# Optimization experiments

Measured on AMD Instinct MI355X. Metric: run time of the kernel, lower is better.

The kernel has to match this reference:

```python
import jax, jax.numpy as jnp
import numpy as np

N, E = 20000, 320000
IN, HID, OUT, EO = 256, 256, 128, 64


def setup_inputs() -> dict:
    key = jax.random.key(0)
    ks = iter(jax.random.split(key, 40))
    w = lambda s: jax.random.normal(next(ks), s, jnp.float32) * 0.05
    inp = {
        "x": jax.random.normal(next(ks), (N, IN), jnp.float32),
        "edge_index": jax.random.randint(next(ks), (2, E), 0, N, jnp.int32),
        "edge_attr": jax.random.uniform(next(ks), (E, 1), jnp.float32),
        # conv1 (IN->IN), conv2 (HID->HID)
        "c1_nw": w((IN, IN)), "c1_ew": w((1, EO)), "c1_new": w((IN + EO, IN)), "c1_b": jnp.zeros((IN,)),
        "c2_nw": w((HID, HID)), "c2_ew": w((1, EO)), "c2_new": w((HID + EO, HID)), "c2_b": jnp.zeros((HID,)),
        # conv3_mean / conv3_logstd (OUT->OUT)
        "cm_nw": w((OUT, OUT)), "cm_ew": w((1, EO)), "cm_new": w((OUT + EO, OUT)), "cm_b": jnp.zeros((OUT,)),
        "cl_nw": w((OUT, OUT)), "cl_ew": w((1, EO)), "cl_new": w((OUT + EO, OUT)), "cl_b": jnp.zeros((OUT,)),
        # linears (stored [in,out])
        "lin1_w": w((IN, HID)), "lin1_b": jnp.zeros((HID,)),
        "lin2_w": w((HID, OUT)), "lin2_b": jnp.zeros((OUT,)),
        "pih_w": w((IN, HID)), "pih_b": jnp.zeros((HID,)),
        "pho_w": w((HID, OUT)), "pho_b": jnp.zeros((OUT,)),
        # batchnorm affine params
        "bn1_g": jnp.ones((IN,)), "bn1_b": jnp.zeros((IN,)),
        "bn2_g": jnp.ones((HID,)), "bn2_b": jnp.zeros((HID,)),
        "bnm_g": jnp.ones((OUT,)), "bnm_b": jnp.zeros((OUT,)),
        "bnl_g": jnp.ones((OUT,)), "bnl_b": jnp.zeros((OUT,)),
    }
    return inp


def _forward(x, edge_index, edge_attr,
             c1_nw, c1_ew, c1_new, c1_b,
             c2_nw, c2_ew, c2_new, c2_b,
             cm_nw, cm_ew, cm_new, cm_b,
             cl_nw, cl_ew, cl_new, cl_b,
             lin1_w, lin1_b, lin2_w, lin2_b,
             pih_w, pih_b, pho_w, pho_b,
             bn1_g, bn1_b, bn2_g, bn2_b,
             bnm_g, bnm_b, bnl_g, bnl_b):
    n = x.shape[0]
    loops = jnp.arange(n, dtype=edge_index.dtype)
    row = jnp.concatenate([edge_index[0], loops])  # source j
    col = jnp.concatenate([edge_index[1], loops])  # target i
    ea = jnp.concatenate([edge_attr, jnp.zeros((n, edge_attr.shape[1]), edge_attr.dtype)], 0)
    deg = jax.ops.segment_sum(jnp.ones_like(col, dtype=x.dtype), col, num_segments=n) + 1e-6
    dis = deg ** -0.5
    norm = dis[row] * dis[col]  # [E+N]

    def gcn(h, nw, ew, new_w, b):
        nm = (h @ nw)[row]                      # gather of x_j @ node_weight
        em = ea @ ew                            # [E+N, EO]
        msg = norm[:, None] * (jnp.concatenate([nm, em], axis=1) @ new_w)
        return jax.ops.segment_sum(msg, col, num_segments=n) + b

    def bn(h, g, b):  # BatchNorm1d, training-mode batch stats, eps 1e-5
        m = h.mean(0)
        v = h.var(0)
        return (h - m) * jax.lax.rsqrt(v + 1e-5) * g + b

    # dropout is identity in eval mode
    x1 = jax.nn.relu(bn(gcn(x, c1_nw, c1_ew, c1_new, c1_b), bn1_g, bn1_b)) + x
    x2 = x1 @ lin1_w + lin1_b
    x2 = jax.nn.relu(bn(gcn(x2, c2_nw, c2_ew, c2_new, c2_b), bn2_g, bn2_b)) + (x1 @ pih_w + pih_b)
    x3 = x2 @ lin2_w + lin2_b
    logstd = bn(gcn(x3, cl_nw, cl_ew, cl_new, cl_b), bnl_g, bnl_b)
    mean = bn(gcn(x3, cm_nw, cm_ew, cm_new, cm_b), bnm_g, bnm_b) + (x2 @ pho_w + pho_b)
    # faithful to source: batch_norm_logstd applied a second time and added
    logstd = logstd + bn(logstd, bnl_g, bnl_b)
    return mean, logstd


def reference(x, edge_index, edge_attr,
              c1_nw, c1_ew, c1_new, c1_b,
              c2_nw, c2_ew, c2_new, c2_b,
              cm_nw, cm_ew, cm_new, cm_b,
              cl_nw, cl_ew, cl_new, cl_b,
              lin1_w, lin1_b, lin2_w, lin2_b,
              pih_w, pih_b, pho_w, pho_b,
              bn1_g, bn1_b, bn2_g, bn2_b,
              bnm_g, bnm_b, bnl_g, bnl_b):
    return _forward(x, edge_index, edge_attr,
                    c1_nw, c1_ew, c1_new, c1_b,
                    c2_nw, c2_ew, c2_new, c2_b,
                    cm_nw, cm_ew, cm_new, cm_b,
                    cl_nw, cl_ew, cl_new, cl_b,
                    lin1_w, lin1_b, lin2_w, lin2_b,
                    pih_w, pih_b, pho_w, pho_b,
                    bn1_g, bn1_b, bn2_g, bn2_b,
                    bnm_g, bnm_b, bnl_g, bnl_b)
```

## Files before the change

### kernel.cpp

```cpp
#include <hip/hip_runtime.h>

#define NN 20000
#define EE 320000
#define ET (EE + NN)

typedef __attribute__((ext_vector_type(8))) short short8v;
typedef __attribute__((ext_vector_type(4))) float float4v;

__device__ __forceinline__ float b2f(unsigned short u) {
  union { float f; unsigned int i; } c; c.i = ((unsigned int)u) << 16; return c.f;
}
__device__ __forceinline__ unsigned short f2bs(float f) {
  union { float f; unsigned int u; } c; c.f = f;
  unsigned int r = c.u + 0x7fffu + ((c.u >> 16) & 1u);
  return (unsigned short)(r >> 16);
}

__global__ void detect_kernel(const unsigned short* __restrict__ x, int* __restrict__ flag) {
  __shared__ int cnt_s;
  if (threadIdx.x == 0) cnt_s = 0;
  __syncthreads();
  int pass = 0;
  for (int j = 0; j < 16; ++j) {
    unsigned short u = x[2 * (threadIdx.x * 16 + j)];
    int e = (u >> 7) & 0xFF;
    if (e >= 96 && e <= 150) pass++;
  }
  atomicAdd(&cnt_s, pass);
  __syncthreads();
  if (threadIdx.x == 0) *flag = (cnt_s < 2458) ? 1 : 0;
}

__global__ void convert_kernel(const void* __restrict__ in, float* __restrict__ out, int n4,
                               const int* __restrict__ flag) {
  int i = blockIdx.x * 256 + threadIdx.x;
  if (i >= n4) return;
  if (*flag) {
    ((float4*)out)[i] = ((const float4*)in)[i];
  } else {
    ushort4 u = ((const ushort4*)in)[i];
    ((float4*)out)[i] = make_float4(b2f(u.x), b2f(u.y), b2f(u.z), b2f(u.w));
  }
}

__global__ void convert_x_kernel(const void* __restrict__ in,
                                 short* __restrict__ xh, short* __restrict__ xl, int n4,
                                 const int* __restrict__ flag) {
  int i = blockIdx.x * 256 + threadIdx.x;
  if (i >= n4) return;
  float4 v;
  if (*flag) {
    v = ((const float4*)in)[i];
  } else {
    ushort4 u = ((const ushort4*)in)[i];
    v = make_float4(b2f(u.x), b2f(u.y), b2f(u.z), b2f(u.w));
  }
  ushort4 h, l;
  h.x = f2bs(v.x); l.x = f2bs(v.x - b2f(h.x));
  h.y = f2bs(v.y); l.y = f2bs(v.y - b2f(h.y));
  h.z = f2bs(v.z); l.z = f2bs(v.z - b2f(h.z));
  h.w = f2bs(v.w); l.w = f2bs(v.w - b2f(h.w));
  ((ushort4*)xh)[i] = h;
  ((ushort4*)xl)[i] = l;
}

struct WSpec { const void* p[28]; int off[28]; int len[28]; };
__global__ void convert_weights(WSpec ws, float* __restrict__ out, const int* __restrict__ flag) {
  int b = blockIdx.x;
  int f32m = *flag;
  const void* p = ws.p[b];
  int off = ws.off[b], len4 = ws.len[b] >> 2;
  float4* dst = (float4*)(out + off);
  for (int i = blockIdx.y * 256 + threadIdx.x; i < len4; i += 8 * 256) {
    if (f32m) {
      dst[i] = ((const float4*)p)[i];
    } else {
      ushort4 u = ((const ushort4*)p)[i];
      dst[i] = make_float4(b2f(u.x), b2f(u.y), b2f(u.z), b2f(u.w));
    }
  }
}

__global__ void bconv_kernel(const float* __restrict__ W, int ldb,
                             short* __restrict__ Bh, short* __restrict__ Bl, int N) {
  int idx = blockIdx.x * 256 + threadIdx.x;
  if (idx >= N * 256) return;
  int n = idx >> 8, k = idx & 255;
  float v = W[(size_t)k * ldb + n];
  unsigned short h = f2bs(v);
  size_t o = ((size_t)(k >> 3) * N + n) * 8 + (k & 7);
  Bh[o] = (short)h;
  Bl[o] = (short)f2bs(v - b2f(h));
}

__global__ void count_kernel(const int* __restrict__ ei, int* __restrict__ cnt) {
  int e = blockIdx.x * 256 + threadIdx.x;
  if (e >= ET) return;
  int dst = (e < EE) ? ei[EE + e] : (e - EE);
  atomicAdd(&cnt[dst], 1);
}

__global__ void dis_kernel(const int* __restrict__ cnt, float* __restrict__ dis) {
  int i = blockIdx.x * 256 + threadIdx.x;
  if (i >= NN) return;
  dis[i] = rsqrtf((float)cnt[i] + 1e-6f);
}

__global__ void scan1_kernel(const int* __restrict__ cnt, int* __restrict__ partial,
                             int* __restrict__ bsum) {
  __shared__ int sd[256];
  int b = blockIdx.x, t = threadIdx.x;
  int i = b * 256 + t;
  sd[t] = (i < NN) ? cnt[i] : 0;
  __syncthreads();
  for (int off = 1; off < 256; off <<= 1) {
    int x = (t >= off) ? sd[t - off] : 0;
    __syncthreads();
    sd[t] += x;
    __syncthreads();
  }
  if (i < NN) partial[i] = sd[t];
  if (t == 255) bsum[b] = sd[255];
}

__global__ void scan2_kernel(int* __restrict__ bsum, int nb) {
  __shared__ int sd[128];
  int t = threadIdx.x;
  sd[t] = (t < nb) ? bsum[t] : 0;
  __syncthreads();
  for (int off = 1; off < 128; off <<= 1) {
    int x = (t >= off) ? sd[t - off] : 0;
    __syncthreads();
    sd[t] += x;
    __syncthreads();
  }
  if (t < nb) bsum[t] = sd[t];
}

__global__ void scan3_kernel(const int* __restrict__ partial, const int* __restrict__ bsum,
                             int* __restrict__ rowptr) {
  int i = blockIdx.x * 256 + threadIdx.x;
  if (i == 0) rowptr[0] = 0;
  if (i < NN) {
    int b = i >> 8;
    rowptr[i + 1] = partial[i] + (b ? bsum[b - 1] : 0);
  }
}

__global__ void fill_kernel(const int* __restrict__ ei, const float* __restrict__ eaf,
                            const float* __restrict__ dis, const int* __restrict__ rowptr,
                            int* __restrict__ cursor, int2* __restrict__ csr,
                            float* __restrict__ sarr) {
  int e = blockIdx.x * 256 + threadIdx.x;
  if (e >= ET) return;
  int src, dst; float a;
  if (e < EE) { src = ei[e]; dst = ei[EE + e]; a = eaf[e]; }
  else { src = dst = e - EE; a = 0.f; }
  float coef = dis[src] * dis[dst];
  int pos = rowptr[dst] + atomicAdd(&cursor[dst], 1);
  csr[pos] = make_int2(src, __float_as_int(coef));
  if (a != 0.f) atomicAdd(&sarr[dst], coef * a);
}

struct GJobs {
  const float* A[8]; const float* B[8]; float* C[8];
  int M[8], N[8], K[8], ldc[8], blkx[8], cum[8];
  int njobs;
};
__global__ __launch_bounds__(256) void gemm64_multi(GJobs jb) {
  int bid = blockIdx.x;
  int j = 0;
  while (j < jb.njobs - 1 && bid >= jb.cum[j]) ++j;
  int local = bid - (j ? jb.cum[j - 1] : 0);
  const float* A = jb.A[j];
  const float* B = jb.B[j];
  float* C = jb.C[j];
  int M = jb.M[j], N = jb.N[j], K = jb.K[j], ldc = jb.ldc[j];
  int bx = local % jb.blkx[j], by = local / jb.blkx[j];

  __shared__ float As[16][68];
  __shared__ float Bs[16][64];
  int tid = threadIdx.x;
  int row0 = bx * 64, col0 = by * 64;
  int tr = tid >> 4, tc = tid & 15;
  float acc[4][4] = {};
  int lmA = tid >> 2;
  int lkA = (tid & 3) << 2;
  int lkB = tid >> 4;
  int lcB = (tid & 15) << 2;
  for (int k0 = 0; k0 < K; k0 += 16) {
    int gr = row0 + lmA;
    float4 a4 = make_float4(0.f, 0.f, 0.f, 0.f);
    if (gr < M) a4 = *reinterpret_cast<const float4*>(&A[(size_t)gr * K + k0 + lkA]);
    As[lkA + 0][lmA] = a4.x;
    As[lkA + 1][lmA] = a4.y;
    As[lkA + 2][lmA] = a4.z;
    As[lkA + 3][lmA] = a4.w;
    float4 b4 = *reinterpret_cast<const float4*>(&B[(size_t)(k0 + lkB) * N + col0 + lcB]);
    *reinterpret_cast<float4*>(&Bs[lkB][lcB]) = b4;
    __syncthreads();
#pragma unroll
    for (int kk = 0; kk < 16; ++kk) {
      float4 av = *reinterpret_cast<const float4*>(&As[kk][tr << 2]);
      float4 bv = *reinterpret_cast<const float4*>(&Bs[kk][tc << 2]);
      float aa[4] = {av.x, av.y, av.z, av.w};
      float bb[4] = {bv.x, bv.y, bv.z, bv.w};
#pragma unroll
      for (int i = 0; i < 4; ++i)
#pragma unroll
        for (int jj = 0; jj < 4; ++jj) acc[i][jj] += aa[i] * bb[jj];
    }
    __syncthreads();
  }
#pragma unroll
  for (int i = 0; i < 4; ++i) {
    int gr = row0 + (tr << 2) + i;
    if (gr >= M) continue;
#pragma unroll
    for (int jj = 0; jj < 4; ++jj)
      C[(size_t)gr * ldc + col0 + (tc << 2) + jj] = acc[i][jj];
  }
}

__global__ void copy_strided(const float* __restrict__ src, float* __restrict__ dst,
                             int n, int cshift, int cmask, int ldd) {
  int idx = blockIdx.x * 256 + threadIdx.x;
  if (idx >= n) return;
  int r = idx >> cshift, c = idx & cmask;
  dst[(size_t)r * ldd + c] = src[idx];
}

#define LOADB(ntv, ktv, BH, BL)                                     \
  {                                                                 \
    int n_ = (ntv) * 128 + w * 16 + lm;                             \
    _Pragma("unroll") for (int ks = 0; ks < 2; ++ks) {              \
      int kc = (ktv) * 8 + ks * 4 + lg;                             \
      size_t o = ((size_t)kc * N + n_) * 8;                         \
      BH[ks] = *reinterpret_cast<const short8v*>(Bh + o);           \
      BL[ks] = *reinterpret_cast<const short8v*>(Bl + o);           \
    }                                                               \
  }

__global__ __launch_bounds__(512) void gemm_mfma4(const short* __restrict__ Ah,
                                                  const short* __restrict__ Al,
                                                  const short* __restrict__ Bh,
                                                  const short* __restrict__ Bl,
                                                  unsigned short* __restrict__ C,
                                                  const float* __restrict__ bias,
                                                  int M, int N, int ldc) {
  __shared__ __align__(16) short lds[16384];
  const int K = 256;
  int tid = threadIdx.x;
  int w = tid >> 6, l = tid & 63;
  int row0 = blockIdx.x * 32;
  int lm = l & 15, lg = l >> 4;

#pragma unroll
  for (int i = 0; i < 2; ++i) {
    int id = i * 512 + tid;
    int r = id >> 5, c = id & 31;
    int gr = row0 + r; if (gr >= M) gr = M - 1;
    int sw = c ^ r;
    *reinterpret_cast<float4*>(lds + r * 256 + sw * 8) =
        *reinterpret_cast<const float4*>(Ah + (size_t)gr * K + c * 8);
    *reinterpret_cast<float4*>(lds + 8192 + r * 256 + sw * 8) =
        *reinterpret_cast<const float4*>(Al + (size_t)gr * K + c * 8);
  }
  __syncthreads();

  int NT = N >> 7;
  short8v bhX[2], blX[2], bhY[2], blY[2];
  LOADB(0, 0, bhX, blX);
  for (int nt = 0; nt < NT; ++nt) {
    float4v acc[2] = {};
    int n = nt * 128 + w * 16 + lm;
#pragma unroll
    for (int kt = 0; kt < 4; ++kt) {
      int nt_n = (kt == 3) ? ((nt + 1 < NT) ? nt + 1 : nt) : nt;
      int kt_n = (kt + 1) & 3;
      short8v a_h[2][2], a_l[2][2];
#pragma unroll
      for (int mf = 0; mf < 2; ++mf)
#pragma unroll
        for (int ks = 0; ks < 2; ++ks) {
          int r = mf * 16 + lm;
          int c = kt * 8 + ks * 4 + lg;
          int sw = c ^ r;
          a_h[mf][ks] = *reinterpret_cast<const short8v*>(lds + r * 256 + sw * 8);
          a_l[mf][ks] = *reinterpret_cast<const short8v*>(lds + 8192 + r * 256 + sw * 8);
        }
      if ((kt & 1) == 0) {
        LOADB(nt_n, kt_n, bhY, blY);
#pragma unroll
        for (int mf = 0; mf < 2; ++mf)
#pragma unroll
          for (int ks = 0; ks < 2; ++ks) {
            acc[mf] = __builtin_amdgcn_mfma_f32_16x16x32_bf16(a_h[mf][ks], bhX[ks], acc[mf], 0, 0, 0);
            acc[mf] = __builtin_amdgcn_mfma_f32_16x16x32_bf16(a_h[mf][ks], blX[ks], acc[mf], 0, 0, 0);
            acc[mf] = __builtin_amdgcn_mfma_f32_16x16x32_bf16(a_l[mf][ks], bhX[ks], acc[mf], 0, 0, 0);
          }
      } else {
        LOADB(nt_n, kt_n, bhX, blX);
#pragma unroll
        for (int mf = 0; mf < 2; ++mf)
#pragma unroll
          for (int ks = 0; ks < 2; ++ks) {
            acc[mf] = __builtin_amdgcn_mfma_f32_16x16x32_bf16(a_h[mf][ks], bhY[ks], acc[mf], 0, 0, 0);
            acc[mf] = __builtin_amdgcn_mfma_f32_16x16x32_bf16(a_h[mf][ks], blY[ks], acc[mf], 0, 0, 0);
            acc[mf] = __builtin_amdgcn_mfma_f32_16x16x32_bf16(a_l[mf][ks], bhY[ks], acc[mf], 0, 0, 0);
          }
      }
    }
    float bb = bias ? bias[n] : 0.f;
#pragma unroll
    for (int mf = 0; mf < 2; ++mf)
#pragma unroll
      for (int r = 0; r < 4; ++r) {
        int m = row0 + mf * 16 + lg * 4 + r;
        if (m < M) C[(size_t)m * ldc + n] = f2bs(acc[mf][r] + bb);
      }
  }
}

__global__ void agg_kernel(const unsigned short* __restrict__ U, int ldu,
                           const int* __restrict__ rowptr, const int2* __restrict__ csr,
                           const float* __restrict__ sarr, const float* __restrict__ V,
                           float* __restrict__ G) {
  int i = blockIdx.x, t = threadIdx.x;
  float s = sarr[i];
  float4 v4 = ((const float4*)V)[t];
  float ax = s * v4.x, ay = s * v4.y, az = s * v4.z, aw = s * v4.w;
  int p1 = rowptr[i + 1];
  for (int p = rowptr[i]; p < p1; ++p) {
    int2 e = csr[p];
    float c = __int_as_float(e.y);
    ushort4 u4 = *reinterpret_cast<const ushort4*>(U + (size_t)e.x * ldu + (t << 2));
    ax += c * b2f(u4.x); ay += c * b2f(u4.y); az += c * b2f(u4.z); aw += c * b2f(u4.w);
  }
  *reinterpret_cast<float4*>(G + (size_t)i * 256 + (t << 2)) = make_float4(ax, ay, az, aw);
}

__global__ void colpart_kernel(const float* __restrict__ h, float* __restrict__ part, int F) {
  __shared__ float4 sm0[256], sm1[256];
  int t = threadIdx.x;
  int cols4 = F >> 2;
  int lc = t & (cols4 - 1);
  int team = t / cols4;
  int rpi = 256 / cols4;
  int r0 = blockIdx.x * 64;
  int r1 = min(r0 + 64, NN);
  float4 s0 = make_float4(0.f, 0.f, 0.f, 0.f);
  float4 s1 = make_float4(0.f, 0.f, 0.f, 0.f);
  for (int r = r0 + team; r < r1; r += rpi) {
    float4 x = *reinterpret_cast<const float4*>(h + (size_t)r * F + lc * 4);
    s0.x += x.x; s0.y += x.y; s0.z += x.z; s0.w += x.w;
    s1.x += x.x * x.x; s1.y += x.y * x.y; s1.z += x.z * x.z; s1.w += x.w * x.w;
  }
  sm0[t] = s0; sm1[t] = s1;
  __syncthreads();
  if (team == 0) {
    for (int k = 1; k < rpi; ++k) {
      float4 a = sm0[k * cols4 + lc];
      float4 b = sm1[k * cols4 + lc];
      s0.x += a.x; s0.y += a.y; s0.z += a.z; s0.w += a.w;
      s1.x += b.x; s1.y += b.y; s1.z += b.z; s1.w += b.w;
    }
    *reinterpret_cast<float4*>(part + (size_t)blockIdx.x * 2 * F + lc * 4) = s0;
    *reinterpret_cast<float4*>(part + (size_t)blockIdx.x * 2 * F + F + lc * 4) = s1;
  }
}

__global__ void bnred_kernel(const float* __restrict__ part, float* __restrict__ part2,
                             int F2, int nb) {
  int c = blockIdx.x * 256 + threadIdx.x;
  if (c >= F2) return;
  int chunk = blockIdx.y;
  int cs = (nb + 7) >> 3;
  int b0 = chunk * cs;
  int b1 = min(b0 + cs, nb);
  float s0 = 0.f, s1 = 0.f, s2 = 0.f, s3 = 0.f;
  int b = b0;
  for (; b + 3 < b1; b += 4) {
    s0 += part[(size_t)(b + 0) * F2 + c];
    s1 += part[(size_t)(b + 1) * F2 + c];
    s2 += part[(size_t)(b + 2) * F2 + c];
    s3 += part[(size_t)(b + 3) * F2 + c];
  }
  for (; b < b1; ++b) s0 += part[(size_t)b * F2 + c];
  part2[(size_t)chunk * F2 + c] = (s0 + s1) + (s2 + s3);
}

__global__ void bnfin_kernel(const float* __restrict__ part2, const float* __restrict__ gamma,
                             const float* __restrict__ beta, int F,
                             float* __restrict__ scsh) {
  int t = threadIdx.x;
  int F2 = 2 * F;
  float s0 = 0.f, s1 = 0.f;
#pragma unroll
  for (int b = 0; b < 8; ++b) {
    s0 += part2[(size_t)b * F2 + t];
    s1 += part2[(size_t)b * F2 + F + t];
  }
  const float invn = 1.f / (float)NN;
  float m = s0 * invn;
  float var = s1 * invn - m * m;
  float sc = gamma[t] * rsqrtf(var + 1e-5f);
  scsh[t] = sc;
  scsh[F + t] = beta[t] - m * sc;
}

__global__ void bnfin2_kernel(const float* __restrict__ part2, const float* __restrict__ scsh,
                              const float* __restrict__ gamma2, const float* __restrict__ beta2,
                              float* __restrict__ ab) {
  int t = threadIdx.x;
  int c = 128 + t;
  float s0 = 0.f, s1 = 0.f;
#pragma unroll
  for (int b = 0; b < 8; ++b) {
    s0 += part2[(size_t)b * 512 + c];
    s1 += part2[(size_t)b * 512 + 256 + c];
  }
  const float invn = 1.f / (float)NN;
  float m_g = s0 * invn;
  float v_g = s1 * invn - m_g * m_g;
  float sc1 = scsh[c];
  float sh1 = scsh[256 + c];
  float m_L = m_g * sc1 + sh1;
  float v_L = v_g * sc1 * sc1;
  float sc2 = gamma2[t] * rsqrtf(v_L + 1e-5f);
  float sh2 = beta2[t] - m_L * sc2;
  ab[t] = sc1 * (1.f + sc2);
  ab[128 + t] = sh1 * (1.f + sc2) + sh2;
}

__global__ void apply_x1_kernel(const float* __restrict__ g, const float* __restrict__ scsh,
                                const short* __restrict__ xh, const short* __restrict__ xl,
                                short* __restrict__ oh, short* __restrict__ ol, int n) {
  int idx = blockIdx.x * 256 + threadIdx.x;
  if (idx >= n) return;
  int c = idx & 255;
  float xr = b2f((unsigned short)xh[idx]) + b2f((unsigned short)xl[idx]);
  float y = fmaxf(g[idx] * scsh[c] + scsh[256 + c], 0.f) + xr;
  unsigned short h = f2bs(y);
  oh[idx] = (short)h;
  ol[idx] = (short)f2bs(y - b2f(h));
}

__global__ void apply_x2_kernel(const float* __restrict__ g, const float* __restrict__ scsh,
                                const unsigned short* __restrict__ ucat, short* __restrict__ oh,
                                short* __restrict__ ol, int n) {
  int idx = blockIdx.x * 256 + threadIdx.x;
  if (idx >= n) return;
  int r = idx >> 8, c = idx & 255;
  float y = fmaxf(g[idx] * scsh[c] + scsh[256 + c], 0.f) + b2f(ucat[(size_t)r * 512 + 256 + c]);
  unsigned short h = f2bs(y);
  oh[idx] = (short)h;
  ol[idx] = (short)f2bs(y - b2f(h));
}

__global__ void apply_mean_kernel(const float* __restrict__ g, const float* __restrict__ scsh,
                                  const unsigned short* __restrict__ ucat, float* __restrict__ out,
                                  int n) {
  int idx = blockIdx.x * 256 + threadIdx.x;
  if (idx >= n) return;
  int r = idx >> 7, c = idx & 127;
  float v = g[(size_t)r * 256 + c];
  out[idx] = v * scsh[c] + scsh[256 + c] + b2f(ucat[(size_t)r * 384 + 256 + c]);
}

__global__ void apply_ln2g_kernel(const float* __restrict__ g, const float* __restrict__ ab,
                                  float* __restrict__ out, int n) {
  int idx = blockIdx.x * 256 + threadIdx.x;
  if (idx >= n) return;
  int r = idx >> 7, c = idx & 127;
  float v = g[(size_t)r * 256 + 128 + c];
  out[idx] = v * ab[c] + ab[128 + c];
}

__global__ void write_code(float* __restrict__ out, float code) {
  int i = blockIdx.x * 256 + threadIdx.x;
  if (i < 4096) out[i] = code;
}

extern "C" void kernel_launch(void* const* d_in, const int* in_sizes, int n_in,
                              void* d_out, int out_size, void* d_ws, size_t ws_size,
                              hipStream_t stream) {
  float* out_mean = (float*)d_out;
  float* out_logstd = out_mean + (size_t)NN * 128;

  static const int expect[35] = {5120000, 640000, 320000,
                                 65536, 64, 81920, 256,  65536, 64, 81920, 256,
                                 16384, 64, 24576, 128,  16384, 64, 24576, 128,
                                 65536, 256, 32768, 128, 65536, 256, 32768, 128,
                                 256, 256, 256, 256, 128, 128, 128, 128};
  if (n_in != 35) { write_code<<<16, 256, 0, stream>>>(out_mean, 900.f); return; }
  if (out_size != 5120000) { write_code<<<16, 256, 0, stream>>>(out_mean, 950.f); return; }
  for (int i = 0; i < 35; ++i)
    if (in_sizes[i] != expect[i]) {
      write_code<<<16, 256, 0, stream>>>(out_mean, 1000.f + 10.f * i);
      return;
    }

  const int* ei = (const int*)d_in[1];

  char* w = (char*)d_ws;
  size_t off = 0;
  auto alloc = [&](size_t bytes) -> void* {
    void* p = w + off;
    off += (bytes + 255) & ~(size_t)255;
    return p;
  };
  int* flag = (int*)alloc(4);
  int* cnt = (int*)alloc(NN * 4);
  int* rowptr = (int*)alloc((NN + 1) * 4);
  int* bsum = (int*)alloc(128 * 4);
  int* spart = (int*)alloc(NN * 4);
  int2* csr = (int2*)alloc((size_t)ET * 8);
  float* dis = (float*)alloc(NN * 4);
  float* sarr = (float*)alloc(NN * 4);
  float* eaf = (float*)alloc((size_t)EE * 4);
  float* Wf = (float*)alloc((size_t)576000 * 4);
  float* W1 = (float*)alloc((size_t)65536 * 4);
  float* W2cat = (float*)alloc((size_t)131072 * 4);
  float* W3cat = (float*)alloc((size_t)98304 * 4);
  float* WCa = (float*)alloc((size_t)65536 * 4);
  float* WCb = (float*)alloc((size_t)16384 * 4);
  float* WCc = (float*)alloc((size_t)16384 * 4);
  float* bias2 = (float*)alloc(512 * 4);
  float* bias3 = (float*)alloc(384 * 4);
  float* V1 = (float*)alloc(256 * 4);
  float* V2 = (float*)alloc(256 * 4);
  float* Vcat3 = (float*)alloc(256 * 4);
  float* Gpart = (float*)alloc((size_t)313 * 512 * 4);
  float* Gpart2 = (float*)alloc((size_t)8 * 512 * 4);
  float* scsh = (float*)alloc(512 * 4);
  float* ab = (float*)alloc(256 * 4);
  short* Bh1 = (short*)alloc((size_t)256 * 256 * 2);
  short* Bl1 = (short*)alloc((size_t)256 * 256 * 2);
  short* Bh2 = (short*)alloc((size_t)512 * 256 * 2);
  short* Bl2 = (short*)alloc((size_t)512 * 256 * 2);
  short* Bh3 = (short*)alloc((size_t)384 * 256 * 2);
  short* Bl3 = (short*)alloc((size_t)384 * 256 * 2);
  float* Gbuf = (float*)alloc((size_t)NN * 256 * 4);
  float* regB = (float*)alloc((size_t)NN * 256 * 4);
  float* regC = (float*)alloc((size_t)NN * 256 * 4);
  float* Ucat = (float*)alloc((size_t)NN * 512 * 4);
  if (off > ws_size) { write_code<<<16, 256, 0, stream>>>(out_mean, 2000.f); return; }

  unsigned short* U1 = (unsigned short*)regB;
  short* X1h = (short*)regB;
  short* X1l = X1h + (size_t)NN * 256;
  short* X2h = X1h;
  short* X2l = X1l;
  short* Xh = (short*)regC;
  short* Xl = Xh + (size_t)NN * 256;
  float* G = Gbuf;
  unsigned short* Ucat_u = (unsigned short*)Ucat;

  const int n256 = NN * 256, n128 = NN * 128;
  const int g256 = (n256 + 255) / 256, g128 = (n128 + 255) / 256;
  const int nb = (NN + 255) / 256;
  const int nbc = (NN + 63) / 64;

  detect_kernel<<<1, 256, 0, stream>>>((const unsigned short*)d_in[0], flag);
  convert_x_kernel<<<(n256 / 4 + 255) / 256, 256, 0, stream>>>(d_in[0], Xh, Xl, n256 / 4, flag);
  convert_kernel<<<(EE / 4 + 255) / 256, 256, 0, stream>>>(d_in[2], eaf, EE / 4, flag);

  WSpec wsp;
  const int map[28] = {3, 5, 7, 9, 11, 13, 15, 17, 4, 8, 12, 16, 19, 21, 23, 25,
                       20, 22, 24, 26, 27, 28, 29, 30, 31, 33, 32, 34};
  const int offs[28] = {0, 65536, 147456, 212992, 294912, 311296, 335872, 352256,
                        376832, 376896, 376960, 377024, 377088, 442624, 475392, 540928,
                        573696, 573952, 574080, 574336, 574464, 574720, 574976, 575232,
                        575488, 575616, 575744, 575872};
  const int lens[28] = {65536, 81920, 65536, 81920, 16384, 24576, 16384, 24576,
                        64, 64, 64, 64, 65536, 32768, 65536, 32768,
                        256, 128, 256, 128, 256, 256, 256, 256,
                        128, 128, 128, 128};
  for (int i = 0; i < 28; ++i) { wsp.p[i] = d_in[map[i]]; wsp.off[i] = offs[i]; wsp.len[i] = lens[i]; }
  convert_weights<<<dim3(28, 8), 256, 0, stream>>>(wsp, Wf, flag);

  hipMemsetAsync(cnt, 0, NN * 4, stream);
  count_kernel<<<(ET + 255) / 256, 256, 0, stream>>>(ei, cnt);
  dis_kernel<<<(NN + 255) / 256, 256, 0, stream>>>(cnt, dis);
  scan1_kernel<<<nb, 256, 0, stream>>>(cnt, spart, bsum);
  scan2_kernel<<<1, 128, 0, stream>>>(bsum, nb);
  scan3_kernel<<<nb, 256, 0, stream>>>(spart, bsum, rowptr);
  hipMemsetAsync(cnt, 0, NN * 4, stream);
  hipMemsetAsync(sarr, 0, NN * 4, stream);
  fill_kernel<<<(ET + 255) / 256, 256, 0, stream>>>(ei, eaf, dis, rowptr, cnt, csr, sarr);

  {
    GJobs jb{};
    auto set = [&](int j, const float* A, const float* B, float* C, int M, int N, int K,
                   int ldc, int bx, int cum) {
      jb.A[j] = A; jb.B[j] = B; jb.C[j] = C; jb.M[j] = M; jb.N[j] = N; jb.K[j] = K;
      jb.ldc[j] = ldc; jb.blkx[j] = bx; jb.cum[j] = cum;
    };
    set(0, Wf + 0,      Wf + 65536,  W1,          256, 256, 256, 256, 4, 16);
    set(1, Wf + 147456, Wf + 212992, WCa,         256, 256, 256, 256, 4, 32);
    set(2, Wf + 294912, Wf + 311296, WCb,         128, 128, 128, 128, 2, 36);
    set(3, Wf + 335872, Wf + 352256, WCc,         128, 128, 128, 128, 2, 40);
    set(4, Wf + 376832, Wf + 131072, V1,          1,   256, 64,  256, 1, 44);
    set(5, Wf + 376896, Wf + 278528, V2,          1,   256, 64,  256, 1, 48);
    set(6, Wf + 376960, Wf + 327680, Vcat3,       1,   128, 64,  128, 1, 50);
    set(7, Wf + 377024, Wf + 368640, Vcat3 + 128, 1,   128, 64,  128, 1, 52);
    jb.njobs = 8;
    gemm64_multi<<<52, 256, 0, stream>>>(jb);
  }
  {
    GJobs jb{};
    auto set = [&](int j, const float* A, const float* B, float* C, int M, int N, int K,
                   int ldc, int bx, int cum) {
      jb.A[j] = A; jb.B[j] = B; jb.C[j] = C; jb.M[j] = M; jb.N[j] = N; jb.K[j] = K;
      jb.ldc[j] = ldc; jb.blkx[j] = bx; jb.cum[j] = cum;
    };
    set(0, Wf + 377088, WCa, W2cat,       256, 256, 256, 512, 4, 16);
    set(1, Wf + 573696, WCa, bias2,       1,   256, 256, 512, 1, 20);
    set(2, Wf + 442624, WCb, W3cat,       256, 128, 128, 384, 4, 28);
    set(3, Wf + 442624, WCc, W3cat + 128, 256, 128, 128, 384, 4, 36);
    set(4, Wf + 573952, WCb, bias3,       1,   128, 128, 384, 1, 38);
    set(5, Wf + 573952, WCc, bias3 + 128, 1,   128, 128, 384, 1, 40);
    jb.njobs = 6;
    gemm64_multi<<<40, 256, 0, stream>>>(jb);
  }
  copy_strided<<<256, 256, 0, stream>>>(Wf + 475392, W2cat + 256, 65536, 8, 255, 512);
  copy_strided<<<1, 256, 0, stream>>>(Wf + 574080, bias2 + 256, 256, 8, 255, 512);
  copy_strided<<<128, 256, 0, stream>>>(Wf + 540928, W3cat + 256, 32768, 7, 127, 384);
  copy_strided<<<1, 256, 0, stream>>>(Wf + 574336, bias3 + 256, 128, 7, 127, 384);

  bconv_kernel<<<256, 256, 0, stream>>>(W1, 256, Bh1, Bl1, 256);
  bconv_kernel<<<512, 256, 0, stream>>>(W2cat, 512, Bh2, Bl2, 512);
  bconv_kernel<<<384, 256, 0, stream>>>(W3cat, 384, Bh3, Bl3, 384);

  gemm_mfma4<<<625, 512, 0, stream>>>(Xh, Xl, Bh1, Bl1, U1, nullptr, NN, 256, 256);
  agg_kernel<<<NN, 64, 0, stream>>>(U1, 256, rowptr, csr, sarr, V1, G);
  colpart_kernel<<<nbc, 256, 0, stream>>>(G, Gpart, 256);
  bnred_kernel<<<dim3(2, 8), 256, 0, stream>>>(Gpart, Gpart2, 512, nbc);
  bnfin_kernel<<<1, 256, 0, stream>>>(Gpart2, Wf + 574464, Wf + 574720, 256, scsh);
  apply_x1_kernel<<<g256, 256, 0, stream>>>(G, scsh, Xh, Xl, X1h, X1l, n256);

  gemm_mfma4<<<625, 512, 0, stream>>>(X1h, X1l, Bh2, Bl2, Ucat_u, bias2, NN, 512, 512);
  agg_kernel<<<NN, 64, 0, stream>>>(Ucat_u, 512, rowptr, csr, sarr, V2, G);
  colpart_kernel<<<nbc, 256, 0, stream>>>(G, Gpart, 256);
  bnred_kernel<<<dim3(2, 8), 256, 0, stream>>>(Gpart, Gpart2, 512, nbc);
  bnfin_kernel<<<1, 256, 0, stream>>>(Gpart2, Wf + 574976, Wf + 575232, 256, scsh);
  apply_x2_kernel<<<g256, 256, 0, stream>>>(G, scsh, Ucat_u, X2h, X2l, n256);

  gemm_mfma4<<<625, 512, 0, stream>>>(X2h, X2l, Bh3, Bl3, Ucat_u, bias3, NN, 384, 384);
  agg_kernel<<<NN, 64, 0, stream>>>(Ucat_u, 384, rowptr, csr, sarr, Vcat3, G);
  colpart_kernel<<<nbc, 256, 0, stream>>>(G, Gpart, 256);
  bnred_kernel<<<dim3(2, 8), 256, 0, stream>>>(Gpart, Gpart2, 512, nbc);
  bnfin_kernel<<<1, 256, 0, stream>>>(Gpart2, Wf + 575488, Wf + 575744, 256, scsh);
  bnfin2_kernel<<<1, 128, 0, stream>>>(Gpart2, scsh, Wf + 575616, Wf + 575872, ab);
  apply_mean_kernel<<<g128, 256, 0, stream>>>(G, scsh, Ucat_u, out_mean, n128);
  apply_ln2g_kernel<<<g128, 256, 0, stream>>>(G, ab, out_logstd, n128);
}
```

Baseline: 391.1 us.

## Fuse BN-apply/ReLU/residual into GEMM A-tile load and drop edge_attr convert

The batchnorm apply, ReLU and residual add that produced X1 and X2 are moved into the A-tile staging of the following MFMA GEMM, which is templated on a mode. This removes two full-size elementwise kernels and their bf16 hi/lo intermediate writes and reads. The edge-attribute conversion kernel is also removed; fill_kernel now reads the raw input and branches on the dtype flag. The cost is more global reads and arithmetic in each GEMM block's prologue, and a third U buffer aliases regB so U2 survives for the layer-3 residual.

```diff
diff --git a/kernel.cpp b/kernel.cpp
--- a/kernel.cpp
+++ b/kernel.cpp
@@ -29,18 +29,6 @@
   atomicAdd(&cnt_s, pass);
   __syncthreads();
   if (threadIdx.x == 0) *flag = (cnt_s < 2458) ? 1 : 0;
-}
-
-__global__ void convert_kernel(const void* __restrict__ in, float* __restrict__ out, int n4,
-                               const int* __restrict__ flag) {
-  int i = blockIdx.x * 256 + threadIdx.x;
-  if (i >= n4) return;
-  if (*flag) {
-    ((float4*)out)[i] = ((const float4*)in)[i];
-  } else {
-    ushort4 u = ((const ushort4*)in)[i];
-    ((float4*)out)[i] = make_float4(b2f(u.x), b2f(u.y), b2f(u.z), b2f(u.w));
-  }
 }
 
 __global__ void convert_x_kernel(const void* __restrict__ in,
@@ -147,15 +135,19 @@
   }
 }
 
-__global__ void fill_kernel(const int* __restrict__ ei, const float* __restrict__ eaf,
+__global__ void fill_kernel(const int* __restrict__ ei, const void* __restrict__ ea,
                             const float* __restrict__ dis, const int* __restrict__ rowptr,
                             int* __restrict__ cursor, int2* __restrict__ csr,
-                            float* __restrict__ sarr) {
+                            float* __restrict__ sarr, const int* __restrict__ flag) {
   int e = blockIdx.x * 256 + threadIdx.x;
   if (e >= ET) return;
   int src, dst; float a;
-  if (e < EE) { src = ei[e]; dst = ei[EE + e]; a = eaf[e]; }
-  else { src = dst = e - EE; a = 0.f; }
+  if (e < EE) {
+    src = ei[e]; dst = ei[EE + e];
+    a = (*flag) ? ((const float*)ea)[e] : b2f(((const unsigned short*)ea)[e]);
+  } else {
+    src = dst = e - EE; a = 0.f;
+  }
   float coef = dis[src] * dis[dst];
   int pos = rowptr[dst] + atomicAdd(&cursor[dst], 1);
   csr[pos] = make_int2(src, __float_as_int(coef));
@@ -241,8 +233,14 @@
     }                                                               \
   }
 
-__global__ __launch_bounds__(512) void gemm_mfma4(const short* __restrict__ Ah,
+template <int MODE>
+__global__ __launch_bounds__(512) void gemm_fused(const short* __restrict__ Ah,
                                                   const short* __restrict__ Al,
+                                                  const float* __restrict__ Gsrc,
+                                                  const float* __restrict__ scshp,
+                                                  const short* __restrict__ Rh,
+                                                  const short* __restrict__ Rl,
+                                                  const unsigned short* __restrict__ ures,
                                                   const short* __restrict__ Bh,
                                                   const short* __restrict__ Bl,
                                                   unsigned short* __restrict__ C,
@@ -261,10 +259,47 @@
     int r = id >> 5, c = id & 31;
     int gr = row0 + r; if (gr >= M) gr = M - 1;
     int sw = c ^ r;
-    *reinterpret_cast<float4*>(lds + r * 256 + sw * 8) =
-        *reinterpret_cast<const float4*>(Ah + (size_t)gr * K + c * 8);
-    *reinterpret_cast<float4*>(lds + 8192 + r * 256 + sw * 8) =
-        *reinterpret_cast<const float4*>(Al + (size_t)gr * K + c * 8);
+    if (MODE == 0) {
+      *reinterpret_cast<float4*>(lds + r * 256 + sw * 8) =
+          *reinterpret_cast<const float4*>(Ah + (size_t)gr * K + c * 8);
+      *reinterpret_cast<float4*>(lds + 8192 + r * 256 + sw * 8) =
+          *reinterpret_cast<const float4*>(Al + (size_t)gr * K + c * 8);
+    } else {
+      const float* gp = Gsrc + (size_t)gr * 256 + c * 8;
+      float4 g0 = *reinterpret_cast<const float4*>(gp);
+      float4 g1 = *reinterpret_cast<const float4*>(gp + 4);
+      float4 sc0 = *reinterpret_cast<const float4*>(scshp + c * 8);
+      float4 sc1 = *reinterpret_cast<const float4*>(scshp + c * 8 + 4);
+      float4 sh0 = *reinterpret_cast<const float4*>(scshp + 256 + c * 8);
+      float4 sh1 = *reinterpret_cast<const float4*>(scshp + 256 + c * 8 + 4);
+      float vals[8] = {g0.x * sc0.x + sh0.x, g0.y * sc0.y + sh0.y,
+                       g0.z * sc0.z + sh0.z, g0.w * sc0.w + sh0.w,
+                       g1.x * sc1.x + sh1.x, g1.y * sc1.y + sh1.y,
+                       g1.z * sc1.z + sh1.z, g1.w * sc1.w + sh1.w};
+      float res[8];
+      if (MODE == 1) {
+        short8v hv = *reinterpret_cast<const short8v*>(Rh + (size_t)gr * 256 + c * 8);
+        short8v lv = *reinterpret_cast<const short8v*>(Rl + (size_t)gr * 256 + c * 8);
+#pragma unroll
+        for (int j = 0; j < 8; ++j)
+          res[j] = b2f((unsigned short)hv[j]) + b2f((unsigned short)lv[j]);
+      } else {
+        short8v uv = *reinterpret_cast<const short8v*>(
+            (const short*)ures + (size_t)gr * 512 + 256 + c * 8);
+#pragma unroll
+        for (int j = 0; j < 8; ++j) res[j] = b2f((unsigned short)uv[j]);
+      }
+      short8v hs, ls;
+#pragma unroll
+      for (int j = 0; j < 8; ++j) {
+        float y = fmaxf(vals[j], 0.f) + res[j];
+        unsigned short h = f2bs(y);
+        hs[j] = (short)h;
+        ls[j] = (short)f2bs(y - b2f(h));
+      }
+      *reinterpret_cast<short8v*>(lds + r * 256 + sw * 8) = hs;
+      *reinterpret_cast<short8v*>(lds + 8192 + r * 256 + sw * 8) = ls;
+    }
   }
   __syncthreads();
 
@@ -433,31 +468,6 @@
   ab[128 + t] = sh1 * (1.f + sc2) + sh2;
 }
 
-__global__ void apply_x1_kernel(const float* __restrict__ g, const float* __restrict__ scsh,
-                                const short* __restrict__ xh, const short* __restrict__ xl,
-                                short* __restrict__ oh, short* __restrict__ ol, int n) {
-  int idx = blockIdx.x * 256 + threadIdx.x;
-  if (idx >= n) return;
-  int c = idx & 255;
-  float xr = b2f((unsigned short)xh[idx]) + b2f((unsigned short)xl[idx]);
-  float y = fmaxf(g[idx] * scsh[c] + scsh[256 + c], 0.f) + xr;
-  unsigned short h = f2bs(y);
-  oh[idx] = (short)h;
-  ol[idx] = (short)f2bs(y - b2f(h));
-}
-
-__global__ void apply_x2_kernel(const float* __restrict__ g, const float* __restrict__ scsh,
-                                const unsigned short* __restrict__ ucat, short* __restrict__ oh,
-                                short* __restrict__ ol, int n) {
-  int idx = blockIdx.x * 256 + threadIdx.x;
-  if (idx >= n) return;
-  int r = idx >> 8, c = idx & 255;
-  float y = fmaxf(g[idx] * scsh[c] + scsh[256 + c], 0.f) + b2f(ucat[(size_t)r * 512 + 256 + c]);
-  unsigned short h = f2bs(y);
-  oh[idx] = (short)h;
-  ol[idx] = (short)f2bs(y - b2f(h));
-}
-
 __global__ void apply_mean_kernel(const float* __restrict__ g, const float* __restrict__ scsh,
                                   const unsigned short* __restrict__ ucat, float* __restrict__ out,
                                   int n) {
@@ -518,7 +528,6 @@
   int2* csr = (int2*)alloc((size_t)ET * 8);
   float* dis = (float*)alloc(NN * 4);
   float* sarr = (float*)alloc(NN * 4);
-  float* eaf = (float*)alloc((size_t)EE * 4);
   float* Wf = (float*)alloc((size_t)576000 * 4);
   float* W1 = (float*)alloc((size_t)65536 * 4);
   float* W2cat = (float*)alloc((size_t)131072 * 4);
@@ -548,23 +557,19 @@
   if (off > ws_size) { write_code<<<16, 256, 0, stream>>>(out_mean, 2000.f); return; }
 
   unsigned short* U1 = (unsigned short*)regB;
-  short* X1h = (short*)regB;
-  short* X1l = X1h + (size_t)NN * 256;
-  short* X2h = X1h;
-  short* X2l = X1l;
+  unsigned short* U3 = (unsigned short*)regB;
   short* Xh = (short*)regC;
   short* Xl = Xh + (size_t)NN * 256;
   float* G = Gbuf;
-  unsigned short* Ucat_u = (unsigned short*)Ucat;
+  unsigned short* U2 = (unsigned short*)Ucat;
 
   const int n256 = NN * 256, n128 = NN * 128;
-  const int g256 = (n256 + 255) / 256, g128 = (n128 + 255) / 256;
+  const int g128 = (n128 + 255) / 256;
   const int nb = (NN + 255) / 256;
   const int nbc = (NN + 63) / 64;
 
   detect_kernel<<<1, 256, 0, stream>>>((const unsigned short*)d_in[0], flag);
   convert_x_kernel<<<(n256 / 4 + 255) / 256, 256, 0, stream>>>(d_in[0], Xh, Xl, n256 / 4, flag);
-  convert_kernel<<<(EE / 4 + 255) / 256, 256, 0, stream>>>(d_in[2], eaf, EE / 4, flag);
 
   WSpec wsp;
   const int map[28] = {3, 5, 7, 9, 11, 13, 15, 17, 4, 8, 12, 16, 19, 21, 23, 25,
@@ -588,7 +593,7 @@
   scan3_kernel<<<nb, 256, 0, stream>>>(spart, bsum, rowptr);
   hipMemsetAsync(cnt, 0, NN * 4, stream);
   hipMemsetAsync(sarr, 0, NN * 4, stream);
-  fill_kernel<<<(ET + 255) / 256, 256, 0, stream>>>(ei, eaf, dis, rowptr, cnt, csr, sarr);
+  fill_kernel<<<(ET + 255) / 256, 256, 0, stream>>>(ei, d_in[2], dis, rowptr, cnt, csr, sarr, flag);
 
   {
     GJobs jb{};
@@ -633,26 +638,27 @@
   bconv_kernel<<<512, 256, 0, stream>>>(W2cat, 512, Bh2, Bl2, 512);
   bconv_kernel<<<384, 256, 0, stream>>>(W3cat, 384, Bh3, Bl3, 384);
 
-  gemm_mfma4<<<625, 512, 0, stream>>>(Xh, Xl, Bh1, Bl1, U1, nullptr, NN, 256, 256);
+  gemm_fused<0><<<625, 512, 0, stream>>>(Xh, Xl, nullptr, nullptr, nullptr, nullptr, nullptr,
+                                         Bh1, Bl1, U1, nullptr, NN, 256, 256);
   agg_kernel<<<NN, 64, 0, stream>>>(U1, 256, rowptr, csr, sarr, V1, G);
   colpart_kernel<<<nbc, 256, 0, stream>>>(G, Gpart, 256);
   bnred_kernel<<<dim3(2, 8), 256, 0, stream>>>(Gpart, Gpart2, 512, nbc);
   bnfin_kernel<<<1, 256, 0, stream>>>(Gpart2, Wf + 574464, Wf + 574720, 256, scsh);
-  apply_x1_kernel<<<g256, 256, 0, stream>>>(G, scsh, Xh, Xl, X1h, X1l, n256);
-
-  gemm_mfma4<<<625, 512, 0, stream>>>(X1h, X1l, Bh2, Bl2, Ucat_u, bias2, NN, 512, 512);
-  agg_kernel<<<NN, 64, 0, stream>>>(Ucat_u, 512, rowptr, csr, sarr, V2, G);
+
+  gemm_fused<1><<<625, 512, 0, stream>>>(nullptr, nullptr, G, scsh, Xh, Xl, nullptr,
+                                         Bh2, Bl2, U2, bias2, NN, 512, 512);
+  agg_kernel<<<NN, 64, 0, stream>>>(U2, 512, rowptr, csr, sarr, V2, G);
   colpart_kernel<<<nbc, 256, 0, stream>>>(G, Gpart, 256);
   bnred_kernel<<<dim3(2, 8), 256, 0, stream>>>(Gpart, Gpart2, 512, nbc);
   bnfin_kernel<<<1, 256, 0, stream>>>(Gpart2, Wf + 574976, Wf + 575232, 256, scsh);
-  apply_x2_kernel<<<g256, 256, 0, stream>>>(G, scsh, Ucat_u, X2h, X2l, n256);
-
-  gemm_mfma4<<<625, 512, 0, stream>>>(X2h, X2l, Bh3, Bl3, Ucat_u, bias3, NN, 384, 384);
-  agg_kernel<<<NN, 64, 0, stream>>>(Ucat_u, 384, rowptr, csr, sarr, Vcat3, G);
+
+  gemm_fused<2><<<625, 512, 0, stream>>>(nullptr, nullptr, G, scsh, nullptr, nullptr, U2,
+                                         Bh3, Bl3, U3, bias3, NN, 384, 384);
+  agg_kernel<<<NN, 64, 0, stream>>>(U3, 384, rowptr, csr, sarr, Vcat3, G);
   colpart_kernel<<<nbc, 256, 0, stream>>>(G, Gpart, 256);
   bnred_kernel<<<dim3(2, 8), 256, 0, stream>>>(Gpart, Gpart2, 512, nbc);
   bnfin_kernel<<<1, 256, 0, stream>>>(Gpart2, Wf + 575488, Wf + 575744, 256, scsh);
   bnfin2_kernel<<<1, 128, 0, stream>>>(Gpart2, scsh, Wf + 575616, Wf + 575872, ab);
-  apply_mean_kernel<<<g128, 256, 0, stream>>>(G, scsh, Ucat_u, out_mean, n128);
+  apply_mean_kernel<<<g128, 256, 0, stream>>>(G, scsh, U3, out_mean, n128);
   apply_ln2g_kernel<<<g128, 256, 0, stream>>>(G, ab, out_logstd, n128);
 }
```

New measurement: 375.0 us. -4.1%, faster.
